# Optimization experiments

Hardware: AMD Instinct MI355X
Metric: run time of the kernel (lower is better)

Reference implementation:

```python
import jax, jax.numpy as jnp
import numpy as np

B, N, IN_DIM, HID, K = 8, 4096, 10, 64, 8
NORM = np.array([1.0/2950.0, 1.0/2950.0, 1.0/2950.0, 1.0/5.265625, 1.0/143.875,
                 1.0/589.0, 1.0/1.2050781, 1.0/211.0, 1.0, 1.0/7.0], dtype=np.float32)


def _lin(key, fan_in, fan_out):
    k1, k2 = jax.random.split(key)
    s = 1.0 / np.sqrt(fan_in)
    w = jax.random.uniform(k1, (fan_in, fan_out), jnp.float32, -s, s)
    b = jax.random.uniform(k2, (fan_out,), jnp.float32, -s, s)
    return w, b


def setup_inputs() -> dict:
    key = jax.random.key(0)
    ks = jax.random.split(key, 10)
    x = jax.random.normal(ks[0], (B, N, IN_DIM), jnp.float32)
    w_in1, b_in1 = _lin(ks[1], IN_DIM, HID // 2)
    w_in2, b_in2 = _lin(ks[2], HID // 2, HID)
    w_c1a, b_c1a = _lin(ks[3], 2 * HID, 3 * HID // 2)
    w_c1b, b_c1b = _lin(ks[4], 3 * HID // 2, HID)
    w_c2a, b_c2a = _lin(ks[5], 2 * HID, 3 * HID // 2)
    w_c2b, b_c2b = _lin(ks[6], 3 * HID // 2, HID)
    w_o1, b_o1 = _lin(ks[7], HID, HID)
    w_o2, b_o2 = _lin(ks[8], HID, HID // 2)
    w_o3, b_o3 = _lin(ks[9], HID // 2, 2)
    return dict(x=x, datanorm=jnp.asarray(NORM),
                w_in1=w_in1, b_in1=b_in1, w_in2=w_in2, b_in2=b_in2,
                w_c1a=w_c1a, b_c1a=b_c1a, w_c1b=w_c1b, b_c1b=b_c1b,
                w_c2a=w_c2a, b_c2a=b_c2a, w_c2b=w_c2b, b_c2b=b_c2b,
                w_o1=w_o1, b_o1=b_o1, w_o2=w_o2, b_o2=b_o2, w_o3=w_o3, b_o3=b_o3)


def _knn(x, k):
    # x: [B, n, H] -> [B, n, k] indices of k nearest neighbors (self excluded)
    x2 = jnp.sum(x * x, -1)
    d = x2[:, :, None] + x2[:, None, :] - 2.0 * jnp.einsum('bnh,bmh->bnm', x, x)
    n = x.shape[1]
    d = d + jnp.eye(n, dtype=x.dtype) * 1e9
    return jax.lax.top_k(-d, k)[1]


def _edge_conv(x, nbr, w1, b1, w2, b2):
    # EdgeConv with max aggregation over undirected kNN edges.
    # message(i <- j) = MLP([x_i, x_j - x_i]); edges symmetrized (j->i and i->j).
    b, n, k = nbr.shape
    dst0 = jnp.broadcast_to(jnp.arange(n)[None, :, None], (b, n, k)).reshape(b, n * k)
    src0 = nbr.reshape(b, n * k)
    src = jnp.concatenate([src0, dst0], 1)  # [b, 2nk]
    dst = jnp.concatenate([dst0, src0], 1)
    xd = jnp.take_along_axis(x, dst[..., None], 1)
    xs = jnp.take_along_axis(x, src[..., None], 1)
    m = jnp.concatenate([xd, xs - xd], -1)           # [b, 2nk, 2H]
    m = jax.nn.elu(m @ w1 + b1)
    m = jax.nn.elu(m @ w2 + b2)
    seg = lambda mm, dd: jax.ops.segment_max(mm, dd, num_segments=n)
    return jax.vmap(seg)(m, dst)                     # [b, n, H]


def reference(x, datanorm, w_in1, b_in1, w_in2, b_in2,
              w_c1a, b_c1a, w_c1b, b_c1b, w_c2a, b_c2a, w_c2b, b_c2b,
              w_o1, b_o1, w_o2, b_o2, w_o3, b_o3):
    h = x * datanorm
    h = jax.nn.elu(h @ w_in1 + b_in1)
    h = jax.nn.elu(h @ w_in2 + b_in2)
    nbr = _knn(jax.lax.stop_gradient(h), K)          # knn_graph is non-differentiable
    h = _edge_conv(h, nbr, w_c1a, b_c1a, w_c1b, b_c1b)
    # deterministic pairwise max-pool (stand-in for graclus+max_pool, halves node count)
    h = h.reshape(B, N // 2, 2, HID).max(2)
    nbr = _knn(jax.lax.stop_gradient(h), K)
    h = _edge_conv(h, nbr, w_c2a, b_c2a, w_c2b, b_c2b)
    # second graclus max_pool_x followed by global_max_pool == global max pool
    g = h.max(1)                                     # [B, HID]
    o = jax.nn.elu(g @ w_o1 + b_o1)
    o = jax.nn.elu(o @ w_o2 + b_o2)
    o = o @ w_o3 + b_o3                              # [B, 2]
    met = jax.nn.softplus(o[:, :1])
    metphi = jnp.pi * (2.0 * jax.nn.sigmoid(o[:, 1:2]) - 1.0)
    return jnp.concatenate([met, metphi], 1)
```

## Files before the change

kernel.cpp:

```cpp
#include <hip/hip_runtime.h>
#include <hip/hip_bf16.h>

#define BATCH 8
#define N1 4096
#define N2 2048
#define HID 64
#define KNN 8
#define INDIM 10

using u64 = unsigned long long;
using bf16 = __hip_bfloat16;
typedef __attribute__((ext_vector_type(8))) short short8;
typedef __attribute__((ext_vector_type(4))) float f32x4;

__device__ __align__(256) float    g_h1[BATCH * N1 * HID];
__device__ __align__(256) float    g_h2[BATCH * N2 * HID];
__device__ __align__(256) float    g_x2n[BATCH * N1];
__device__ __align__(256) float    g_x2n2[BATCH * N2];
__device__ __align__(256) int      g_nbr[BATCH * N1 * KNN];
__device__ __align__(256) float    g_uu[BATCH * N1 * 96];
__device__ __align__(256) float    g_vv[BATCH * N1 * 96];
__device__ __align__(256) unsigned g_ek1[BATCH * N1 * HID];
__device__ __align__(256) unsigned g_ek2[BATCH * N2 * HID];
__device__ __align__(256) short    g_f1[BATCH * N1 * HID];
__device__ __align__(256) short    g_f2[BATCH * N1 * HID];
__device__ __align__(256) short    g_f3[BATCH * N1 * HID];
__device__ __align__(256) float    g_uf[BATCH * N1 * 96];
__device__ __align__(256) float    g_vf[BATCH * N1 * 96];
__device__ __align__(256) short    g_wf1[2 * 4 * 3 * 64 * 8];
__device__ __align__(256) short    g_wf2[2 * 4 * 3 * 64 * 8];

__device__ __forceinline__ float eluf(float x) { return x > 0.f ? x : __expf(x) - 1.f; }
__device__ __forceinline__ unsigned encf(float f) {
  unsigned u = __float_as_uint(f);
  return u ^ ((unsigned)((int)u >> 31) | 0x80000000u);
}
__device__ __forceinline__ float decf(unsigned k) {
  unsigned u = (k & 0x80000000u) ? (k & 0x7FFFFFFFu) : ~k;
  return __uint_as_float(u);
}
#define ENC_NEG1 0x407FFFFFu
__device__ __forceinline__ unsigned enc_safe(float v) {
  if (!(v == v)) return ENC_NEG1;
  return encf(v);
}
__device__ __forceinline__ float dec_safe(unsigned k) {
  float v = decf(k);
  if (!(v == v)) return -1.0f;
  return fminf(fmaxf(v, -3.0e38f), 3.0e38f);
}
__device__ __forceinline__ unsigned umed3(unsigned a, unsigned b, unsigned c) {
  unsigned d;
  asm("v_med3_u32 %0, %1, %2, %3" : "=v"(d) : "v"(a), "v"(b), "v"(c));
  return d;
}
__device__ __forceinline__ void split3(float v, short& b1, short& b2, short& b3) {
  bf16 x1 = __float2bfloat16(v);
  float r1 = v - __bfloat162float(x1);
  bf16 x2 = __float2bfloat16(r1);
  float r2 = r1 - __bfloat162float(x2);
  bf16 x3 = __float2bfloat16(r2);
  b1 = *(short*)&x1; b2 = *(short*)&x2; b3 = *(short*)&x3;
}
__device__ __forceinline__ void split2(float v, short& b1, short& b2) {
  bf16 x1 = __float2bfloat16(v);
  float r1 = v - __bfloat162float(x1);
  bf16 x2 = __float2bfloat16(r1);
  b1 = *(short*)&x1; b2 = *(short*)&x2;
}
__device__ __forceinline__ void store_frags(int node, const short* s1,
                                            const short* s2, const short* s3) {
  size_t tb = ((size_t)(node >> 4)) * 1024 + (node & 15) * 8;
#pragma unroll
  for (int chunk = 0; chunk < 2; ++chunk) {
#pragma unroll
    for (int q = 0; q < 4; ++q) {
      size_t a = tb + chunk * 512 + q * 128;
      int k = chunk * 32 + q * 8;
      *(short8*)(g_f1 + a) = *(const short8*)(s1 + k);
      *(short8*)(g_f2 + a) = *(const short8*)(s2 + k);
      *(short8*)(g_f3 + a) = *(const short8*)(s3 + k);
    }
  }
}
__device__ __forceinline__ void tv_frag(float4 a0, float4 a1, float4 b0,
                                        float4 b1, short8& s1, short8& s2) {
  float v[8] = {a0.x + b0.x, a0.y + b0.y, a0.z + b0.z, a0.w + b0.w,
                a1.x + b1.x, a1.y + b1.y, a1.z + b1.z, a1.w + b1.w};
#pragma unroll
  for (int e = 0; e < 8; ++e) {
    float t = eluf(v[e]);
    short p1, p2;
    split2(t, p1, p2);
    s1[e] = p1; s2[e] = p2;
  }
}

__global__ __launch_bounds__(256) void init_kernel() {
  int t = blockIdx.x * 256 + threadIdx.x;
  uint4 z = make_uint4(ENC_NEG1, ENC_NEG1, ENC_NEG1, ENC_NEG1);
  const int n1 = BATCH * N1 * HID / 4;
  if (t < n1) ((uint4*)g_ek1)[t] = z;
  else ((uint4*)g_ek2)[t - n1] = z;
}

__global__ __launch_bounds__(256) void wfrag_kernel(const float* __restrict__ w1,
                                                    const float* __restrict__ w2) {
  int level = blockIdx.x;
  const float* w = level ? w2 : w1;
  for (int idx = threadIdx.x; idx < 6144; idx += 256) {
    int no = idx / 1536;
    int rem = idx - no * 1536;
    int kc = rem / 512;
    int rem2 = rem - kc * 512;
    int lane = rem2 >> 3;
    int j = rem2 & 7;
    int k = kc * 32 + (lane >> 4) * 8 + j;
    int o = no * 16 + (lane & 15);
    short b1, b2;
    split2(w[k * 64 + o], b1, b2);
    g_wf1[level * 6144 + idx] = b1;
    g_wf2[level * 6144 + idx] = b2;
  }
}

__global__ __launch_bounds__(256) void input_mlp(
    const float* __restrict__ x, const float* __restrict__ norm,
    const float* __restrict__ w1g, const float* __restrict__ b1g,
    const float* __restrict__ w2g, const float* __restrict__ b2g) {
  __shared__ float sw1[320], sb1[32], sw2[2048], sb2[64], snorm[INDIM];
  int t = threadIdx.x;
  for (int q = t; q < 320; q += 256) sw1[q] = w1g[q];
  for (int q = t; q < 2048; q += 256) sw2[q] = w2g[q];
  if (t < 32) sb1[t] = b1g[t];
  if (t < 64) sb2[t] = b2g[t];
  if (t < INDIM) snorm[t] = norm[t];
  __syncthreads();
  int node = blockIdx.x * 256 + t;
  float xv[INDIM];
#pragma unroll
  for (int d = 0; d < INDIM; ++d)
    xv[d] = x[(size_t)node * INDIM + d] * snorm[d];
  float t1[32];
#pragma unroll
  for (int c = 0; c < 32; ++c) {
    float acc = sb1[c];
#pragma unroll
    for (int d = 0; d < INDIM; ++d) acc += xv[d] * sw1[d * 32 + c];
    t1[c] = eluf(acc);
  }
  float* hr = g_h1 + (size_t)node * HID;
  float sq = 0.f;
  short s1l[HID], s2l[HID], s3l[HID];
#pragma unroll
  for (int c = 0; c < HID; ++c) {
    float acc = sb2[c];
#pragma unroll
    for (int d = 0; d < 32; ++d) acc += t1[d] * sw2[d * HID + c];
    float v = eluf(acc);
    hr[c] = v;
    sq += v * v;
    split3(v, s1l[c], s2l[c], s3l[c]);
  }
  store_frags(node, s1l, s2l, s3l);
  g_x2n[node] = sq;
}

template <int LEVEL>
__global__ __launch_bounds__(256, 2) void knn_kernel() {
  constexpr int n = LEVEL ? N2 : N1;
  constexpr int NT = n / 16;
  constexpr int HT = NT / 2;
  constexpr int NSET = LEVEL ? 1 : 2;
  constexpr int SS = NSET * 16;
  __shared__ __align__(16) unsigned char smem[32 * 293 * 4 + 32 * 75 * 8];
  unsigned* lm = (unsigned*)smem;
  u64* mb = (u64*)(smem + 32 * 293 * 4);
  u64* mb2 = (u64*)smem;

  int b = blockIdx.x & 7;
  int rb = (blockIdx.x >> 3) * (2 * SS);
  int t = threadIdx.x;
  int wv = t >> 6, lane = t & 63;
  int s = wv >> 1, hf = wv & 1;
  int q = lane >> 4, c = lane & 15;
  const float* __restrict__ x2b = (LEVEL ? g_x2n2 : g_x2n) + (size_t)b * n;
  size_t abase = ((size_t)((b * n + rb + s * SS) >> 4)) * 1024 + lane * 8;
  short8 A1a[NSET], A1b[NSET], A2a[NSET], A2b[NSET], A3a[NSET], A3b[NSET];
#pragma unroll
  for (int e = 0; e < NSET; ++e) {
    size_t ab = abase + (size_t)e * 1024;
    A1a[e] = *(const short8*)(g_f1 + ab);
    A1b[e] = *(const short8*)(g_f1 + ab + 512);
    A2a[e] = *(const short8*)(g_f2 + ab);
    A2b[e] = *(const short8*)(g_f2 + ab + 512);
    A3a[e] = *(const short8*)(g_f3 + ab);
    A3b[e] = *(const short8*)(g_f3 + ab + 512);
  }
  unsigned best[NSET][4][KNN];
#pragma unroll
  for (int e = 0; e < NSET; ++e)
#pragma unroll
    for (int r = 0; r < 4; ++r)
#pragma unroll
      for (int p = 0; p < KNN; ++p) best[e][r][p] = 0xFFFFFFFFu;
  const int ct0 = hf * HT;
  const int selftile = (rb + s * SS) >> 4;
  const f32x4 zero = {0.f, 0.f, 0.f, 0.f};
  size_t bb = ((size_t)(b * n) >> 4) * 1024 + (size_t)ct0 * 1024 + lane * 8;
  for (int ct = ct0; ct < ct0 + HT; ++ct, bb += 1024) {
    short8 B1a = *(const short8*)(g_f1 + bb);
    short8 B1b = *(const short8*)(g_f1 + bb + 512);
    short8 B2a = *(const short8*)(g_f2 + bb);
    short8 B2b = *(const short8*)(g_f2 + bb + 512);
    short8 B3a = *(const short8*)(g_f3 + bb);
    short8 B3b = *(const short8*)(g_f3 + bb + 512);
    float x2c = x2b[ct * 16 + c];
#pragma unroll
    for (int e = 0; e < NSET; ++e) {
      f32x4 acc0 = __builtin_amdgcn_mfma_f32_16x16x32_bf16(A1a[e], B1a, zero, 0, 0, 0);
      f32x4 acc1 = __builtin_amdgcn_mfma_f32_16x16x32_bf16(A1b[e], B1b, zero, 0, 0, 0);
      acc0 = __builtin_amdgcn_mfma_f32_16x16x32_bf16(A1a[e], B2a, acc0, 0, 0, 0);
      acc1 = __builtin_amdgcn_mfma_f32_16x16x32_bf16(A1b[e], B2b, acc1, 0, 0, 0);
      acc0 = __builtin_amdgcn_mfma_f32_16x16x32_bf16(A2a[e], B1a, acc0, 0, 0, 0);
      acc1 = __builtin_amdgcn_mfma_f32_16x16x32_bf16(A2b[e], B1b, acc1, 0, 0, 0);
      acc0 = __builtin_amdgcn_mfma_f32_16x16x32_bf16(A1a[e], B3a, acc0, 0, 0, 0);
      acc1 = __builtin_amdgcn_mfma_f32_16x16x32_bf16(A1b[e], B3b, acc1, 0, 0, 0);
      acc0 = __builtin_amdgcn_mfma_f32_16x16x32_bf16(A2a[e], B2a, acc0, 0, 0, 0);
      acc1 = __builtin_amdgcn_mfma_f32_16x16x32_bf16(A2b[e], B2b, acc1, 0, 0, 0);
      acc0 = __builtin_amdgcn_mfma_f32_16x16x32_bf16(A3a[e], B1a, acc0, 0, 0, 0);
      acc1 = __builtin_amdgcn_mfma_f32_16x16x32_bf16(A3b[e], B1b, acc1, 0, 0, 0);
      unsigned ck[4];
#pragma unroll
      for (int r = 0; r < 4; ++r) {
        float sm2 = acc0[r] + acc1[r];
        float dd = __builtin_fmaf(-2.f, sm2, x2c);
        ck[r] = (encf(dd) & 0xFFFFFF00u) | (unsigned)ct;
      }
      if (ct == selftile + e) {
#pragma unroll
        for (int r = 0; r < 4; ++r)
          if (c == q * 4 + r) ck[r] = 0xFFFFFFFFu;
      }
#pragma unroll
      for (int r = 0; r < 4; ++r) {
        unsigned x = ck[r];
#pragma unroll
        for (int p = KNN - 1; p >= 1; --p)
          best[e][r][p] = umed3(best[e][r][p - 1], best[e][r][p], x);
        best[e][r][0] = min(best[e][r][0], x);
      }
    }
  }
#pragma unroll
  for (int pass = 0; pass < NSET; ++pass) {
#pragma unroll
    for (int r = 0; r < 4; ++r) {
      int lrow = s * 16 + q * 4 + r;
      unsigned* dst = lm + lrow * 293 + (hf * 16 + c) * 9;
#pragma unroll
      for (int p = 0; p < KNN; ++p) dst[p] = best[pass][r][p];
    }
    __syncthreads();
    {
      int arow = t >> 3, am = t & 7;
      const unsigned* l0 = lm + arow * 293 + (am * 4) * 9;
      u64 fin[KNN];
#pragma unroll
      for (int p = 0; p < KNN; ++p)
        fin[p] = (((u64)l0[p]) << 4) | (unsigned)((am * 4) & 15);
      for (int d = 1; d < 4; ++d) {
        const unsigned* ld = lm + arow * 293 + (am * 4 + d) * 9;
        unsigned cb = (unsigned)((am * 4 + d) & 15);
        for (int p = 0; p < KNN; ++p) {
          u64 ckk = (((u64)ld[p]) << 4) | cb;
          if (ckk >= fin[KNN - 1]) break;
#pragma unroll
          for (int p2 = 0; p2 < KNN; ++p2) {
            u64 ob = fin[p2];
            bool ex = ob < ckk;
            fin[p2] = ex ? ob : ckk;
            ckk = ex ? ckk : ob;
          }
        }
      }
      u64* dst = mb + arow * 75 + am * 9;
#pragma unroll
      for (int p = 0; p < KNN; ++p) dst[p] = fin[p];
    }
    __syncthreads();
    if (t < 64) {
      int brow = t >> 1, bm = t & 1;
      const u64* l0 = mb + brow * 75 + (bm * 4) * 9;
      u64 fin[KNN];
#pragma unroll
      for (int p = 0; p < KNN; ++p) fin[p] = l0[p];
      for (int d = 1; d < 4; ++d) {
        const u64* ld = mb + brow * 75 + (bm * 4 + d) * 9;
        for (int p = 0; p < KNN; ++p) {
          u64 ckk = ld[p];
          if (ckk >= fin[KNN - 1]) break;
#pragma unroll
          for (int p2 = 0; p2 < KNN; ++p2) {
            u64 ob = fin[p2];
            bool ex = ob < ckk;
            fin[p2] = ex ? ob : ckk;
            ckk = ex ? ckk : ob;
          }
        }
      }
      u64* dst = mb2 + (brow * 2 + bm) * 9;
#pragma unroll
      for (int p = 0; p < KNN; ++p) dst[p] = fin[p];
    }
    __syncthreads();
    if (t < 32) {
      int crow = t;
      const u64* l0 = mb2 + (crow * 2) * 9;
      const u64* l1 = mb2 + (crow * 2 + 1) * 9;
      u64 fin[KNN];
#pragma unroll
      for (int p = 0; p < KNN; ++p) fin[p] = l0[p];
      for (int p = 0; p < KNN; ++p) {
        u64 ckk = l1[p];
        if (ckk >= fin[KNN - 1]) break;
#pragma unroll
        for (int p2 = 0; p2 < KNN; ++p2) {
          u64 ob = fin[p2];
          bool ex = ob < ckk;
          fin[p2] = ex ? ob : ckk;
          ckk = ex ? ckk : ob;
        }
      }
      int row = rb + (crow >> 4) * SS + pass * 16 + (crow & 15);
      int* ob = g_nbr + ((size_t)b * n + row) * KNN;
#pragma unroll
      for (int p = 0; p < KNN; ++p) {
        int j = (int)((fin[p] >> 4) & 255u) * 16 + (int)(fin[p] & 15u);
        ob[p] = j & (n - 1);
      }
    }
    if (pass + 1 < NSET) __syncthreads();
  }
}

__global__ __launch_bounds__(256) void uv_kernel(int level,
                                                 const float* __restrict__ w1g,
                                                 const float* __restrict__ b1g) {
  __shared__ float sw1[128 * 96];
  __shared__ float sb1[96];
  int t = threadIdx.x;
  for (int q = t; q < 128 * 96; q += 256) sw1[q] = w1g[q];
  if (t < 96) sb1[t] = b1g[t];
  __syncthreads();
  const int n = level ? N2 : N1;
  const float* h = level ? g_h2 : g_h1;
  int b = blockIdx.x & 7;
  int nl = (blockIdx.x >> 3) * 64 + (t & 63);
  int c0 = (t >> 6) * 24;
  size_t node = (size_t)b * n + nl;
  const float4* h4 = (const float4*)(h + node * HID);
  float hv[HID];
#pragma unroll
  for (int q = 0; q < 16; ++q) {
    float4 vv = h4[q];
    hv[4 * q] = vv.x; hv[4 * q + 1] = vv.y; hv[4 * q + 2] = vv.z; hv[4 * q + 3] = vv.w;
  }
  float ua[24], va[24];
#pragma unroll
  for (int c = 0; c < 24; ++c) { ua[c] = 0.f; va[c] = 0.f; }
  for (int d = 0; d < HID; ++d) {
    float hd = hv[d];
    const float* wt = sw1 + d * 96 + c0;
    const float* wb = sw1 + (HID + d) * 96 + c0;
#pragma unroll
    for (int c = 0; c < 24; ++c) {
      ua[c] += hd * wt[c];
      va[c] += hd * wb[c];
    }
  }
  float* ur = g_uu + node * 96 + c0;
  float* vr = g_vv + node * 96 + c0;
#pragma unroll
  for (int c = 0; c < 24; ++c) {
    float uval = ua[c] - va[c] + sb1[c0 + c];
    float vval = va[c];
    ur[c] = uval;
    vr[c] = vval;
    int kk = c0 + c;
    size_t fa = (node >> 4) * 1536 + (size_t)((kk >> 5) * 512 +
                ((kk >> 3) & 3) * 128 + (nl & 15) * 8 + (kk & 7));
    g_uf[fa] = uval;
    g_vf[fa] = vval;
  }
}

template <int LEVEL>
__global__ __launch_bounds__(256, 1) void edge_kernel(
    const float* __restrict__ b2g) {
  constexpr int n = LEVEL ? N2 : N1;
  unsigned* ekey = LEVEL ? g_ek2 : g_ek1;
  int b = blockIdx.x & 7;
  int t = threadIdx.x;
  int wv = t >> 6, lane = t & 63;
  int q = lane >> 4, c = lane & 15;
  int base16 = (blockIdx.x >> 3) * 64 + wv * 16;
  int node_c = base16 + c;
  const int* nbb = g_nbr + (size_t)b * n * KNN;
  const float* ub = g_uu + (size_t)b * n * 96;
  const float* vb = g_vv + (size_t)b * n * 96;
  size_t ftile = ((size_t)(b * n + base16) >> 4) * 1536;
  unsigned* eb = ekey + (size_t)b * n * HID;
  short8 W1f[4][3], W2f[4][3];
#pragma unroll
  for (int no = 0; no < 4; ++no)
#pragma unroll
    for (int kc = 0; kc < 3; ++kc) {
      int off = LEVEL * 6144 + ((no * 3 + kc) * 64 + lane) * 8;
      W1f[no][kc] = *(const short8*)(g_wf1 + off);
      W2f[no][kc] = *(const short8*)(g_wf2 + off);
    }
  float biasv[4];
#pragma unroll
  for (int no = 0; no < 4; ++no) biasv[no] = b2g[no * 16 + c];
  float macc[16];
#pragma unroll
  for (int e = 0; e < 16; ++e) macc[e] = -1.0f;
  for (int slot = 0; slot < KNN; ++slot) {
    int jn = nbb[(size_t)node_c * KNN + slot] & (n - 1);
    short8 t1[3], t2[3], r1[3], r2[3];
#pragma unroll
    for (int kc = 0; kc < 3; ++kc) {
      size_t fo = ftile + kc * 512 + lane * 8;
      float4 su0 = *(const float4*)(g_uf + fo);
      float4 su1 = *(const float4*)(g_uf + fo + 4);
      float4 sv0 = *(const float4*)(g_vf + fo);
      float4 sv1 = *(const float4*)(g_vf + fo + 4);
      size_t go = (size_t)jn * 96 + kc * 32 + q * 8;
      float4 gv0 = *(const float4*)(vb + go);
      float4 gv1 = *(const float4*)(vb + go + 4);
      float4 gu0 = *(const float4*)(ub + go);
      float4 gu1 = *(const float4*)(ub + go + 4);
      tv_frag(su0, su1, gv0, gv1, t1[kc], t2[kc]);
      tv_frag(gu0, gu1, sv0, sv1, r1[kc], r2[kc]);
    }
    f32x4 aF[4], aR[4];
#pragma unroll
    for (int no = 0; no < 4; ++no) {
      aF[no] = (f32x4){0.f, 0.f, 0.f, 0.f};
      aR[no] = (f32x4){0.f, 0.f, 0.f, 0.f};
    }
#pragma unroll
    for (int no = 0; no < 4; ++no)
#pragma unroll
      for (int kc = 0; kc < 3; ++kc) {
        aF[no] = __builtin_amdgcn_mfma_f32_16x16x32_bf16(t1[kc], W1f[no][kc], aF[no], 0, 0, 0);
        aF[no] = __builtin_amdgcn_mfma_f32_16x16x32_bf16(t2[kc], W1f[no][kc], aF[no], 0, 0, 0);
        aF[no] = __builtin_amdgcn_mfma_f32_16x16x32_bf16(t1[kc], W2f[no][kc], aF[no], 0, 0, 0);
        aR[no] = __builtin_amdgcn_mfma_f32_16x16x32_bf16(r1[kc], W1f[no][kc], aR[no], 0, 0, 0);
        aR[no] = __builtin_amdgcn_mfma_f32_16x16x32_bf16(r2[kc], W1f[no][kc], aR[no], 0, 0, 0);
        aR[no] = __builtin_amdgcn_mfma_f32_16x16x32_bf16(r1[kc], W2f[no][kc], aR[no], 0, 0, 0);
      }
#pragma unroll
    for (int r = 0; r < 4; ++r) {
      int jr = nbb[(size_t)(base16 + q * 4 + r) * KNN + slot] & (n - 1);
#pragma unroll
      for (int no = 0; no < 4; ++no) {
        float mv = eluf(aR[no][r] + biasv[no]);
        atomicMax(&eb[(size_t)jr * HID + no * 16 + c], enc_safe(mv));
      }
    }
#pragma unroll
    for (int no = 0; no < 4; ++no)
#pragma unroll
      for (int r = 0; r < 4; ++r)
        macc[no * 4 + r] = fmaxf(macc[no * 4 + r], eluf(aF[no][r] + biasv[no]));
  }
#pragma unroll
  for (int r = 0; r < 4; ++r) {
    size_t ib = (size_t)(base16 + q * 4 + r) * HID;
#pragma unroll
    for (int no = 0; no < 4; ++no)
      atomicMax(&eb[ib + no * 16 + c], enc_safe(macc[no * 4 + r]));
  }
}

__global__ __launch_bounds__(256) void pool_kernel() {
  int node = blockIdx.x * 256 + threadIdx.x;
  int b = node >> 11;
  int m = node & (N2 - 1);
  const unsigned* e = g_ek1 + ((size_t)b * N1 + 2 * m) * HID;
  float* hr = g_h2 + (size_t)node * HID;
  float sq = 0.f;
  short s1l[HID], s2l[HID], s3l[HID];
#pragma unroll
  for (int d = 0; d < HID; ++d) {
    float mx = fmaxf(dec_safe(e[d]), dec_safe(e[HID + d]));
    hr[d] = mx;
    sq += mx * mx;
    split3(mx, s1l[d], s2l[d], s3l[d]);
  }
  store_frags(node, s1l, s2l, s3l);
  g_x2n2[node] = sq;
}

__global__ __launch_bounds__(256) void final_kernel(
    const float* __restrict__ wo1, const float* __restrict__ bo1,
    const float* __restrict__ wo2, const float* __restrict__ bo2,
    const float* __restrict__ wo3, const float* __restrict__ bo3,
    float* __restrict__ out) {
  __shared__ unsigned red[4][HID];
  __shared__ float g[HID];
  __shared__ float o1s[HID];
  __shared__ float o2s[32];
  int b = blockIdx.x;
  int t = threadIdx.x;
  int grp = t >> 6, d = t & 63;
  const unsigned* e = g_ek2 + (size_t)b * N2 * HID;
  unsigned mk = 0u;
  for (int m = grp; m < N2; m += 4) {
    unsigned qv = e[(size_t)m * HID + d];
    mk = qv > mk ? qv : mk;
  }
  red[grp][d] = mk;
  __syncthreads();
  if (t < HID) {
    unsigned q1 = red[0][t] > red[1][t] ? red[0][t] : red[1][t];
    unsigned q2 = red[2][t] > red[3][t] ? red[2][t] : red[3][t];
    g[t] = dec_safe(q1 > q2 ? q1 : q2);
  }
  __syncthreads();
  if (t < HID) {
    float a1 = bo1[t];
    for (int dd = 0; dd < HID; ++dd) a1 += g[dd] * wo1[dd * HID + t];
    o1s[t] = eluf(a1);
  }
  __syncthreads();
  if (t < 32) {
    float a2 = bo2[t];
    for (int dd = 0; dd < HID; ++dd) a2 += o1s[dd] * wo2[dd * 32 + t];
    o2s[t] = eluf(a2);
  }
  __syncthreads();
  if (t == 0) {
    float acc0 = bo3[0];
    float acc1 = bo3[1];
    for (int dd = 0; dd < 32; ++dd) {
      acc0 += o2s[dd] * wo3[dd * 2 + 0];
      acc1 += o2s[dd] * wo3[dd * 2 + 1];
    }
    float met = fmaxf(acc0, 0.f) + log1pf(expf(-fabsf(acc0)));
    float phi = 3.14159265358979f * (2.f / (1.f + expf(-acc1)) - 1.f);
    out[b * 2 + 0] = met;
    out[b * 2 + 1] = phi;
  }
}

extern "C" void kernel_launch(void* const* d_in, const int* in_sizes, int n_in,
                              void* d_out, int out_size, void* d_ws,
                              size_t ws_size, hipStream_t stream) {
  const float* x     = (const float*)d_in[0];
  const float* dnorm = (const float*)d_in[1];
  const float* w_in1 = (const float*)d_in[2];
  const float* b_in1 = (const float*)d_in[3];
  const float* w_in2 = (const float*)d_in[4];
  const float* b_in2 = (const float*)d_in[5];
  const float* w_c1a = (const float*)d_in[6];
  const float* b_c1a = (const float*)d_in[7];
  const float* w_c1b = (const float*)d_in[8];
  const float* b_c1b = (const float*)d_in[9];
  const float* w_c2a = (const float*)d_in[10];
  const float* b_c2a = (const float*)d_in[11];
  const float* w_c2b = (const float*)d_in[12];
  const float* b_c2b = (const float*)d_in[13];
  const float* w_o1  = (const float*)d_in[14];
  const float* b_o1  = (const float*)d_in[15];
  const float* w_o2  = (const float*)d_in[16];
  const float* b_o2  = (const float*)d_in[17];
  const float* w_o3  = (const float*)d_in[18];
  const float* b_o3  = (const float*)d_in[19];

  init_kernel<<<(BATCH * N1 * HID + BATCH * N2 * HID) / 4 / 256, 256, 0,
                stream>>>();
  wfrag_kernel<<<2, 256, 0, stream>>>(w_c1b, w_c2b);
  input_mlp<<<BATCH * N1 / 256, 256, 0, stream>>>(x, dnorm, w_in1, b_in1,
                                                  w_in2, b_in2);
  knn_kernel<0><<<8 * (N1 / 64), 256, 0, stream>>>();
  uv_kernel<<<8 * (N1 / 64), 256, 0, stream>>>(0, w_c1a, b_c1a);
  edge_kernel<0><<<8 * (N1 / 64), 256, 0, stream>>>(b_c1b);
  pool_kernel<<<BATCH * N2 / 256, 256, 0, stream>>>();
  knn_kernel<1><<<8 * (N2 / 32), 256, 0, stream>>>();
  uv_kernel<<<8 * (N2 / 64), 256, 0, stream>>>(1, w_c2a, b_c2a);
  edge_kernel<1><<<8 * (N2 / 64), 256, 0, stream>>>(b_c2b);
  final_kernel<<<BATCH, 256, 0, stream>>>(w_o1, b_o1, w_o2, b_o2, w_o3, b_o3,
                                          (float*)d_out);
}
```

Before: 574.7 us.

## Shrink kNN merge shared memory in place and raise occupancy target to four blocks

The kNN kernel's top-k merge scratch is collapsed into one shared buffer. Merged 64-bit candidates are written back in place as pairs of 32-bit words instead of into separate u64 staging buffers, which cuts shared memory per block. Launch bounds are raised from 2 to 4 blocks per CU so more waves can hide latency. The stricter bound may force register spilling, since the kernel holds large per-thread best-lists and MFMA fragments.

Result: slower. 790.2 us (+37.5%).

```diff
diff --git a/kernel.cpp b/kernel.cpp
--- a/kernel.cpp
+++ b/kernel.cpp
@@ -167,16 +167,13 @@
 }
 
 template <int LEVEL>
-__global__ __launch_bounds__(256, 2) void knn_kernel() {
+__global__ __launch_bounds__(256, 4) void knn_kernel() {
   constexpr int n = LEVEL ? N2 : N1;
   constexpr int NT = n / 16;
   constexpr int HT = NT / 2;
   constexpr int NSET = LEVEL ? 1 : 2;
   constexpr int SS = NSET * 16;
-  __shared__ __align__(16) unsigned char smem[32 * 293 * 4 + 32 * 75 * 8];
-  unsigned* lm = (unsigned*)smem;
-  u64* mb = (u64*)(smem + 32 * 293 * 4);
-  u64* mb2 = (u64*)smem;
+  __shared__ unsigned lm[32 * 289];
 
   int b = blockIdx.x & 7;
   int rb = (blockIdx.x >> 3) * (2 * SS);
@@ -257,20 +254,21 @@
 #pragma unroll
     for (int r = 0; r < 4; ++r) {
       int lrow = s * 16 + q * 4 + r;
-      unsigned* dst = lm + lrow * 293 + (hf * 16 + c) * 9;
+      unsigned* dst = lm + lrow * 289 + (hf * 16 + c) * 9;
 #pragma unroll
       for (int p = 0; p < KNN; ++p) dst[p] = best[pass][r][p];
     }
     __syncthreads();
     {
       int arow = t >> 3, am = t & 7;
-      const unsigned* l0 = lm + arow * 293 + (am * 4) * 9;
+      unsigned* base = lm + arow * 289;
+      const unsigned* l0 = base + (am * 4) * 9;
       u64 fin[KNN];
 #pragma unroll
       for (int p = 0; p < KNN; ++p)
         fin[p] = (((u64)l0[p]) << 4) | (unsigned)((am * 4) & 15);
       for (int d = 1; d < 4; ++d) {
-        const unsigned* ld = lm + arow * 293 + (am * 4 + d) * 9;
+        const unsigned* ld = base + (am * 4 + d) * 9;
         unsigned cb = (unsigned)((am * 4 + d) & 15);
         for (int p = 0; p < KNN; ++p) {
           u64 ckk = (((u64)ld[p]) << 4) | cb;
@@ -284,21 +282,28 @@
           }
         }
       }
-      u64* dst = mb + arow * 75 + am * 9;
-#pragma unroll
-      for (int p = 0; p < KNN; ++p) dst[p] = fin[p];
+      unsigned* dst = base + (am * 4) * 9;
+#pragma unroll
+      for (int p = 0; p < KNN; ++p) {
+        dst[2 * p] = (unsigned)fin[p];
+        dst[2 * p + 1] = (unsigned)(fin[p] >> 32);
+      }
     }
     __syncthreads();
     if (t < 64) {
       int brow = t >> 1, bm = t & 1;
-      const u64* l0 = mb + brow * 75 + (bm * 4) * 9;
+      unsigned* base = lm + brow * 289;
       u64 fin[KNN];
-#pragma unroll
-      for (int p = 0; p < KNN; ++p) fin[p] = l0[p];
+      {
+        const unsigned* s0 = base + (bm * 4) * 36;
+#pragma unroll
+        for (int p = 0; p < KNN; ++p)
+          fin[p] = (((u64)s0[2 * p + 1]) << 32) | s0[2 * p];
+      }
       for (int d = 1; d < 4; ++d) {
-        const u64* ld = mb + brow * 75 + (bm * 4 + d) * 9;
+        const unsigned* sd = base + (bm * 4 + d) * 36;
         for (int p = 0; p < KNN; ++p) {
-          u64 ckk = ld[p];
+          u64 ckk = (((u64)sd[2 * p + 1]) << 32) | sd[2 * p];
           if (ckk >= fin[KNN - 1]) break;
 #pragma unroll
           for (int p2 = 0; p2 < KNN; ++p2) {
@@ -309,20 +314,23 @@
           }
         }
       }
-      u64* dst = mb2 + (brow * 2 + bm) * 9;
-#pragma unroll
-      for (int p = 0; p < KNN; ++p) dst[p] = fin[p];
+      unsigned* dst = base + (bm * 4) * 36;
+#pragma unroll
+      for (int p = 0; p < KNN; ++p) {
+        dst[2 * p] = (unsigned)fin[p];
+        dst[2 * p + 1] = (unsigned)(fin[p] >> 32);
+      }
     }
     __syncthreads();
     if (t < 32) {
-      int crow = t;
-      const u64* l0 = mb2 + (crow * 2) * 9;
-      const u64* l1 = mb2 + (crow * 2 + 1) * 9;
+      unsigned* base = lm + t * 289;
       u64 fin[KNN];
 #pragma unroll
-      for (int p = 0; p < KNN; ++p) fin[p] = l0[p];
+      for (int p = 0; p < KNN; ++p)
+        fin[p] = (((u64)base[2 * p + 1]) << 32) | base[2 * p];
+      const unsigned* s1 = base + 144;
       for (int p = 0; p < KNN; ++p) {
-        u64 ckk = l1[p];
+        u64 ckk = (((u64)s1[2 * p + 1]) << 32) | s1[2 * p];
         if (ckk >= fin[KNN - 1]) break;
 #pragma unroll
         for (int p2 = 0; p2 < KNN; ++p2) {
@@ -332,7 +340,7 @@
           ckk = ex ? ckk : ob;
         }
       }
-      int row = rb + (crow >> 4) * SS + pass * 16 + (crow & 15);
+      int row = rb + (t >> 4) * SS + pass * 16 + (t & 15);
       int* ob = g_nbr + ((size_t)b * n + row) * KNN;
 #pragma unroll
       for (int p = 0; p < KNN; ++p) {
```
